# Kernel tuning notes

Hardware: AMD Instinct MI355X
Metric: run time of the kernel (lower is better)

The kernel has to match this reference:

```python
import jax, jax.numpy as jnp
import numpy as np

EMBED_DIM = 1024


def setup_inputs() -> dict:
    key = jax.random.key(0)
    ks = jax.random.split(key, 7)
    B, S, D = 4, 2048, EMBED_DIM
    scale = 1.0 / np.sqrt(D)
    x = jax.random.normal(ks[0], (B, S, D), dtype=jnp.float32)
    # nn.Linear weights stored as [out, in]; we keep [in, out] for x @ W
    Wq = jax.random.normal(ks[1], (D, D), dtype=jnp.float32) * scale
    bq = jax.random.normal(ks[2], (D,), dtype=jnp.float32) * scale
    Wk = jax.random.normal(ks[3], (D, D), dtype=jnp.float32) * scale
    bk = jax.random.normal(ks[4], (D,), dtype=jnp.float32) * scale
    Wv = jax.random.normal(ks[5], (D, D), dtype=jnp.float32) * scale
    bv = jax.random.normal(ks[6], (D,), dtype=jnp.float32) * scale
    return {"x": x, "Wq": Wq, "bq": bq, "Wk": Wk, "bk": bk, "Wv": Wv, "bv": bv}


def reference(x, Wq, bq, Wk, bk, Wv, bv):
    # Single-head attention (num_heads unused in original module).
    q = x @ Wq + bq            # [B, S, D]
    k = x @ Wk + bk            # [B, S, D]
    v = x @ Wv + bv            # [B, S, D]
    inv_sqrt_d = 1.0 / jnp.sqrt(jnp.asarray(x.shape[-1], x.dtype))
    scores = jnp.einsum("bsd,btd->bst", q, k) * inv_sqrt_d  # [B, S, S]
    attn = jax.nn.softmax(scores, axis=-1)
    return jnp.einsum("bst,btd->bsd", attn, v)
```

## Files before the change

kernel.cpp:

```cpp
#include <hip/hip_runtime.h>
#include <hip/hip_bf16.h>


using floatx4 = __attribute__((ext_vector_type(4))) float;
using shortx8 = __attribute__((ext_vector_type(8))) short;
using shortx4 = __attribute__((ext_vector_type(4))) short;

__device__ __forceinline__ short f2bf(float f) {
    __hip_bfloat16 h = __float2bfloat16(f);
    return *reinterpret_cast<short*>(&h);
}
__device__ __forceinline__ float bf2f(short s) {
    unsigned u = (unsigned)(unsigned short)s << 16;
    return __uint_as_float(u);
}

#define MFMA16(a, b, c) __builtin_amdgcn_mfma_f32_16x16x32_bf16((a), (b), (c), 0, 0, 0)

__device__ __forceinline__ void gld_lds16(const void* g, void* l) {
    __builtin_amdgcn_global_load_lds(
        (const __attribute__((address_space(1))) void*)g,
        (__attribute__((address_space(3))) void*)l, 16, 0, 0);
}

template<int MH>
__device__ __forceinline__ void rdA(const short* sAb, int wm, int lrow,
                                    int xo0, int xo1, shortx8 (&af)[4][2]) {
    const short* base = sAb + ((wm << 7) + (MH << 6) + lrow) * 64;
#pragma unroll
    for (int i = 0; i < 4; ++i) {
        af[i][0] = *reinterpret_cast<const shortx8*>(base + i * 1024 + xo0);
        af[i][1] = *reinterpret_cast<const shortx8*>(base + i * 1024 + xo1);
    }
}
template<int NH>
__device__ __forceinline__ void rdB(const short* sBb, int wn, int lrow,
                                    int xo0, int xo1, shortx8 (&bf)[4][2]) {
    const short* base = sBb + ((wn << 6) + (NH << 5) + lrow) * 64;
#pragma unroll
    for (int j = 0; j < 2; ++j) {
        bf[NH * 2 + j][0] = *reinterpret_cast<const shortx8*>(base + j * 1024 + xo0);
        bf[NH * 2 + j][1] = *reinterpret_cast<const shortx8*>(base + j * 1024 + xo1);
    }
}
template<int MH, int NH>
__device__ __forceinline__ void mfq(shortx8 (&af)[4][2], shortx8 (&bf)[4][2],
                                    floatx4 (&acc)[8][4]) {
    __builtin_amdgcn_s_setprio(1);
#pragma unroll
    for (int i = 0; i < 4; ++i) {
#pragma unroll
        for (int j = 0; j < 2; ++j) {
            acc[MH * 4 + i][NH * 2 + j] =
                MFMA16(af[i][0], bf[NH * 2 + j][0], acc[MH * 4 + i][NH * 2 + j]);
            acc[MH * 4 + i][NH * 2 + j] =
                MFMA16(af[i][1], bf[NH * 2 + j][1], acc[MH * 4 + i][NH * 2 + j]);
        }
    }
    __builtin_amdgcn_s_setprio(0);
}

__device__ __forceinline__ void gemm256_loop8(
    const short* __restrict__ A, const short* __restrict__ B,
    int lda, int ldb, int K,
    short* sA, short* sB, floatx4 (&acc)[8][4], int t)
{
    const int w = t >> 6, l = t & 63;
    const int wm = w >> 2, wn = w & 3;
    const int lrow = l & 15, quad = l >> 4, r8 = lrow & 7;
    const int xo0 = (quad ^ r8) << 3;
    const int xo1 = ((quad + 4) ^ r8) << 3;
    const int rr = t >> 3;
    const int gsw = ((t & 7) ^ (rr & 7)) << 3;
    const short* gA0 = A + (size_t)rr * lda + gsw;
    const short* gA1 = A + (size_t)(128 + rr) * lda + gsw;
    const short* gB0 = B + (size_t)rr * ldb + gsw;
    const short* gB1 = B + (size_t)(128 + rr) * ldb + gsw;
    const int wofs = w << 9;

    auto stage = [&](const short* g, int ld, int kt, short* ldsb) {
        const short* p = g + kt;
        gld_lds16(p, ldsb + wofs);
        gld_lds16(p + (size_t)(ld << 6), ldsb + wofs + 4096);
    };

    shortx8 af[4][2], bf[4][2];
    const int NT = K >> 6;

    stage(gA0, lda, 0, sA);
    stage(gA1, lda, 0, sA + 8192);
    stage(gB0, ldb, 0, sB);
    stage(gB1, ldb, 0, sB + 8192);
    stage(gB0, ldb, 64, sB + 16384);
    stage(gB1, ldb, 64, sB + 16384 + 8192);
    asm volatile("s_waitcnt vmcnt(4)" ::: "memory");
    __builtin_amdgcn_s_barrier();

    for (int T = 0; T < NT; T += 2) {
        const bool more = (T + 2) < NT;
        const int ktA1 = (T + 1) << 6;
        const int ktN2 = (T + 2) << 6;
        const int ktB3 = (T + 3) << 6;
        short* sA0 = sA;           short* sB0 = sB;
        short* sA1 = sA + 16384;   short* sB1 = sB + 16384;

        rdA<0>(sA0, wm, lrow, xo0, xo1, af);
        rdB<0>(sB0, wn, lrow, xo0, xo1, bf);
        stage(gA0, lda, ktA1, sA1);
        asm volatile("s_waitcnt lgkmcnt(8)" ::: "memory");
        __builtin_amdgcn_s_barrier();
        asm volatile("s_waitcnt lgkmcnt(0)" ::: "memory");
        __builtin_amdgcn_sched_barrier(0);
        mfq<0, 0>(af, bf, acc);
        __builtin_amdgcn_s_barrier();
        rdB<1>(sB0, wn, lrow, xo0, xo1, bf);
        stage(gA1, lda, ktA1, sA1 + 8192);
        __builtin_amdgcn_s_barrier();
        asm volatile("s_waitcnt lgkmcnt(0)" ::: "memory");
        __builtin_amdgcn_sched_barrier(0);
        mfq<0, 1>(af, bf, acc);
        __builtin_amdgcn_s_barrier();
        rdA<1>(sA0, wm, lrow, xo0, xo1, af);
        if (more) stage(gB0, ldb, ktN2, sB0);
        __builtin_amdgcn_s_barrier();
        asm volatile("s_waitcnt lgkmcnt(0)" ::: "memory");
        __builtin_amdgcn_sched_barrier(0);
        mfq<1, 0>(af, bf, acc);
        __builtin_amdgcn_s_barrier();
        if (more) stage(gB1, ldb, ktN2, sB0 + 8192);
        __builtin_amdgcn_s_barrier();
        __builtin_amdgcn_sched_barrier(0);
        mfq<1, 1>(af, bf, acc);
        if (more) { asm volatile("s_waitcnt vmcnt(4)" ::: "memory"); }
        else      { asm volatile("s_waitcnt vmcnt(0)" ::: "memory"); }
        __builtin_amdgcn_s_barrier();

        rdA<0>(sA1, wm, lrow, xo0, xo1, af);
        rdB<0>(sB1, wn, lrow, xo0, xo1, bf);
        if (more) stage(gA0, lda, ktN2, sA0);
        asm volatile("s_waitcnt lgkmcnt(8)" ::: "memory");
        __builtin_amdgcn_s_barrier();
        asm volatile("s_waitcnt lgkmcnt(0)" ::: "memory");
        __builtin_amdgcn_sched_barrier(0);
        mfq<0, 0>(af, bf, acc);
        __builtin_amdgcn_s_barrier();
        rdB<1>(sB1, wn, lrow, xo0, xo1, bf);
        if (more) stage(gA1, lda, ktN2, sA0 + 8192);
        __builtin_amdgcn_s_barrier();
        asm volatile("s_waitcnt lgkmcnt(0)" ::: "memory");
        __builtin_amdgcn_sched_barrier(0);
        mfq<0, 1>(af, bf, acc);
        __builtin_amdgcn_s_barrier();
        rdA<1>(sA1, wm, lrow, xo0, xo1, af);
        if (more) stage(gB0, ldb, ktB3, sB1);
        __builtin_amdgcn_s_barrier();
        asm volatile("s_waitcnt lgkmcnt(0)" ::: "memory");
        __builtin_amdgcn_sched_barrier(0);
        mfq<1, 0>(af, bf, acc);
        __builtin_amdgcn_s_barrier();
        if (more) stage(gB1, ldb, ktB3, sB1 + 8192);
        __builtin_amdgcn_s_barrier();
        __builtin_amdgcn_sched_barrier(0);
        mfq<1, 1>(af, bf, acc);
        if (more) { asm volatile("s_waitcnt vmcnt(4)" ::: "memory"); }
        __builtin_amdgcn_s_barrier();
    }
}

__device__ __forceinline__ void gemm_loop(
    const short* __restrict__ A, const short* __restrict__ B,
    size_t lda, size_t ldb, int K,
    short* as_, short* bs_, floatx4 (&acc)[4][4], int w, int l)
{
    const int lr8 = l >> 3;
    const int swz = ((l & 7) ^ lr8) * 8;
    const int lrow = l & 15, quad = l >> 4;
    const int wr = w >> 1, wc = w & 1;
    const int r8r = lrow & 7;
    const short* pa = A + (size_t)(w * 32 + lr8) * lda + swz;
    const short* pb = B + (size_t)(w * 32 + lr8) * ldb + swz;
    short* la = as_ + w * 4 * 512;
    short* lb = bs_ + w * 4 * 512;

    for (int kt = 0; kt < K; kt += 64) {
        for (int c = 0; c < 4; ++c) {
            gld_lds16(pa + (size_t)c * 8 * lda + kt, la + c * 512);
            gld_lds16(pb + (size_t)c * 8 * ldb + kt, lb + c * 512);
        }
        __syncthreads();
        for (int kk = 0; kk < 64; kk += 32) {
            const int xoff = (((kk >> 3) + quad) ^ r8r) << 3;
            shortx8 af[4], bfr[4];
            for (int i = 0; i < 4; ++i)
                af[i] = *reinterpret_cast<const shortx8*>(
                    &as_[(size_t)(wr * 64 + i * 16 + lrow) * 64 + xoff]);
            for (int j = 0; j < 4; ++j)
                bfr[j] = *reinterpret_cast<const shortx8*>(
                    &bs_[(size_t)(wc * 64 + j * 16 + lrow) * 64 + xoff]);
            for (int i = 0; i < 4; ++i)
                for (int j = 0; j < 4; ++j)
                    acc[i][j] = MFMA16(af[i], bfr[j], acc[i][j]);
        }
        __syncthreads();
    }
}

__global__ __launch_bounds__(256) void prep_kernel(
    const float* __restrict__ X,
    const float* __restrict__ Wq, const float* __restrict__ Wk,
    const float* __restrict__ Wv,
    const float* __restrict__ bq, const float* __restrict__ bk,
    const float* __restrict__ bv,
    short* __restrict__ Xb, short* __restrict__ Wt,
    float* __restrict__ bcat, float* __restrict__ sums)
{
    const int id = blockIdx.x, t = threadIdx.x;
    if (id < 4096) {
        size_t i = ((size_t)id * 256 + t) * 8;
        float4 v0 = *reinterpret_cast<const float4*>(X + i);
        float4 v1 = *reinterpret_cast<const float4*>(X + i + 4);
        shortx8 s;
        s[0] = f2bf(v0.x); s[1] = f2bf(v0.y); s[2] = f2bf(v0.z); s[3] = f2bf(v0.w);
        s[4] = f2bf(v1.x); s[5] = f2bf(v1.y); s[6] = f2bf(v1.z); s[7] = f2bf(v1.w);
        *reinterpret_cast<shortx8*>(Xb + i) = s;
    } else if (id < 4864) {
        __shared__ float tl[64][65];
        const int wid = id - 4096;
        const int z = wid >> 8, t16 = wid & 255;
        const float* src = (z == 0) ? Wq : (z == 1) ? Wk : Wv;
        short* dst = Wt + (size_t)z * 1024 * 1024;
        const int k0 = (t16 >> 4) * 64, n0 = (t16 & 15) * 64;
        for (int i = t; i < 64 * 64; i += 256) {
            int r = i >> 6, c = i & 63;
            tl[r][c] = src[(size_t)(k0 + r) * 1024 + n0 + c];
        }
        __syncthreads();
        for (int i = t; i < 64 * 64; i += 256) {
            int r = i >> 6, c = i & 63;
            dst[(size_t)(n0 + r) * 1024 + k0 + c] = f2bf(tl[c][r]);
        }
    } else if (id < 4867) {
        const int z = id - 4864;
        const float* bsrc = (z == 0) ? bq : (z == 1) ? bk : bv;
        for (int i = t; i < 1024; i += 256) bcat[z * 1024 + i] = bsrc[i];
    } else {
        const int sid = id - 4867;
        *reinterpret_cast<float4*>(&sums[sid * 1024 + t * 4]) =
            float4{0.f, 0.f, 0.f, 0.f};
    }
}

__global__ __launch_bounds__(512, 2) void qkv_qk_kernel(
    const short* __restrict__ Xb, const short* __restrict__ Wt,
    const float* __restrict__ bcat, short* __restrict__ dQ,
    short* __restrict__ dK)
{
    __shared__ short sA[2 * 16384];
    __shared__ short sB[2 * 16384];
    const int t = threadIdx.x;
    const int m0 = blockIdx.x * 256, n0 = blockIdx.y * 256;
    const int w = t >> 6, l = t & 63;
    const int wm = w >> 2, wn = w & 3, lrow = l & 15, quad = l >> 4;
    const int sec = n0 >> 10;

    floatx4 acc[8][4];
#pragma unroll
    for (int i = 0; i < 8; ++i)
#pragma unroll
        for (int j = 0; j < 4; ++j) acc[i][j] = floatx4{0.f, 0.f, 0.f, 0.f};

    gemm256_loop8(Xb + (size_t)m0 * 1024, Wt + (size_t)n0 * 1024,
                  1024, 1024, 1024, sA, sB, acc, t);

    short* outN = (sec == 0) ? dQ : dK;
#pragma unroll
    for (int i = 0; i < 8; ++i) {
        int rbase = m0 + wm * 128 + i * 16 + quad * 4;
#pragma unroll
        for (int j = 0; j < 4; ++j) {
            int coln = n0 + wn * 64 + j * 16 + lrow;
            int col = coln & 1023;
            float bvv = bcat[coln];
#pragma unroll
            for (int r = 0; r < 4; ++r)
                outN[(size_t)(rbase + r) * 1024 + col] =
                    f2bf(acc[i][j][r] + bvv);
        }
    }
}

__global__ __launch_bounds__(256) void qkv_v_kernel(
    const short* __restrict__ Xb, const short* __restrict__ Wt,
    const float* __restrict__ bcat, short* __restrict__ Vt)
{
    __shared__ short as_[128 * 64];
    __shared__ short bs_[128 * 64];
    const int t = threadIdx.x, w = t >> 6, l = t & 63;
    const int m0 = blockIdx.x * 128;
    const int n0 = 2048 + blockIdx.y * 128;
    const int wr = w >> 1, wc = w & 1, lrow = l & 15, quad = l >> 4;

    floatx4 acc[4][4];
    for (int i = 0; i < 4; ++i)
        for (int j = 0; j < 4; ++j) acc[i][j] = floatx4{0.f, 0.f, 0.f, 0.f};

    gemm_loop(Xb + (size_t)m0 * 1024, Wt + (size_t)n0 * 1024,
              1024, 1024, 1024, as_, bs_, acc, w, l);

    for (int i = 0; i < 4; ++i) {
        int rbase = m0 + wr * 64 + i * 16 + quad * 4;
        int b = rbase >> 11, sl = rbase & 2047;
        for (int j = 0; j < 4; ++j) {
            int coln = n0 + wc * 64 + j * 16 + lrow;
            int col = coln & 1023;
            float bvv = bcat[coln];
            shortx4 s;
            for (int r = 0; r < 4; ++r) s[r] = f2bf(acc[i][j][r] + bvv);
            *reinterpret_cast<shortx4*>(
                &Vt[((size_t)b * 1024 + col) * 2048 + sl]) = s;
        }
    }
}

__global__ __launch_bounds__(512, 2) void scores_kernel(
    const short* __restrict__ dQ, const short* __restrict__ dK,
    short* __restrict__ P, float* __restrict__ sums, int row_start)
{
    __shared__ short sA[2 * 16384];
    __shared__ short sB[2 * 16384];
    const int t = threadIdx.x;
    const int m0 = blockIdx.x * 256;
    const int n0 = blockIdx.y * 256;
    const int g0 = row_start + m0;
    const int b = g0 >> 11;
    const int w = t >> 6, l = t & 63;
    const int wm = w >> 2, wn = w & 3, lrow = l & 15, quad = l >> 4;

    floatx4 acc[8][4];
#pragma unroll
    for (int i = 0; i < 8; ++i)
#pragma unroll
        for (int j = 0; j < 4; ++j) acc[i][j] = floatx4{0.f, 0.f, 0.f, 0.f};

    gemm256_loop8(dQ + (size_t)g0 * 1024, dK + ((size_t)b * 2048 + n0) * 1024,
                  1024, 1024, 1024, sA, sB, acc, t);

#pragma unroll
    for (int i = 0; i < 8; ++i) {
        int rloc = m0 + wm * 128 + i * 16 + quad * 4;
        float rs[4] = {0.f, 0.f, 0.f, 0.f};
#pragma unroll
        for (int j = 0; j < 4; ++j) {
            int col = n0 + wn * 64 + j * 16 + lrow;
#pragma unroll
            for (int r = 0; r < 4; ++r) {
                short pb = f2bf(__expf(acc[i][j][r] * 0.03125f - 20.0f));
                P[(size_t)(rloc + r) * 2048 + col] = pb;
                rs[r] += bf2f(pb);
            }
        }
#pragma unroll
        for (int r = 0; r < 4; ++r)
            for (int m = 1; m <= 8; m <<= 1)
                rs[r] += __shfl_xor(rs[r], m, 64);
        if (lrow == 0)
#pragma unroll
            for (int r = 0; r < 4; ++r)
                atomicAdd(&sums[row_start + rloc + r], rs[r]);
    }
}

__global__ __launch_bounds__(256) void pv_kernel(
    const short* __restrict__ P, const short* __restrict__ Vt,
    const float* __restrict__ sums, float* __restrict__ Out, int row_start)
{
    __shared__ short as_[128 * 64];
    __shared__ short bs_[128 * 64];
    const int t = threadIdx.x, w = t >> 6, l = t & 63;
    const int m0 = blockIdx.x * 128;
    const int n0 = blockIdx.y * 128;
    const int g0 = row_start + m0;
    const int b = g0 >> 11;
    const int wr = w >> 1, wc = w & 1, lrow = l & 15, quad = l >> 4;

    floatx4 acc[4][4];
    for (int i = 0; i < 4; ++i)
        for (int j = 0; j < 4; ++j) acc[i][j] = floatx4{0.f, 0.f, 0.f, 0.f};

    gemm_loop(P + (size_t)m0 * 2048, Vt + ((size_t)b * 1024 + n0) * 2048,
              2048, 2048, 2048, as_, bs_, acc, w, l);

    for (int i = 0; i < 4; ++i) {
        int rloc = m0 + wr * 64 + i * 16 + quad * 4;
        int rglb = row_start + rloc;
        float is[4];
        for (int r = 0; r < 4; ++r) is[r] = 1.0f / sums[rglb + r];
        for (int j = 0; j < 4; ++j) {
            int col = n0 + wc * 64 + j * 16 + lrow;
            for (int r = 0; r < 4; ++r)
                Out[(size_t)(rglb + r) * 1024 + col] = acc[i][j][r] * is[r];
        }
    }
}

extern "C" void kernel_launch(void* const* d_in, const int* in_sizes, int n_in,
                              void* d_out, int out_size, void* d_ws, size_t ws_size,
                              hipStream_t stream)
{
    const float* x  = (const float*)d_in[0];
    const float* Wq = (const float*)d_in[1];
    const float* bq = (const float*)d_in[2];
    const float* Wk = (const float*)d_in[3];
    const float* bk = (const float*)d_in[4];
    const float* Wv = (const float*)d_in[5];
    const float* bv = (const float*)d_in[6];
    float* out = (float*)d_out;

    short* dQ = (short*)d_out;
    short* dK = dQ + (size_t)8192 * 1024;

    char* ws = (char*)d_ws;
    short* Wt   = (short*)ws;
    float* bcat = (float*)(ws + 6291456);
    float* sums = (float*)(ws + 6291456 + 12288);
    short* Vt   = (short*)(ws + 6291456 + 12288 + 32768);
    char*  region = ws + 6291456 + 12288 + 32768 + 16777216;
    const size_t base = 6291456 + 12288 + 32768 + 16777216;

    size_t avail = ws_size > base ? ws_size - base : 0;
    long rows_fit = (long)(avail / 4096);
    int chunk = (int)(rows_fit & ~255L);
    if (chunk > 8192) chunk = 8192;
    if (chunk < 256) chunk = 256;
    short* Xb = (short*)region;
    short* P  = (short*)region;

    prep_kernel<<<dim3(4875), 256, 0, stream>>>(x, Wq, Wk, Wv, bq, bk, bv,
                                                Xb, Wt, bcat, sums);
    qkv_qk_kernel<<<dim3(32, 8), 512, 0, stream>>>(Xb, Wt, bcat, dQ, dK);
    qkv_v_kernel<<<dim3(64, 8), 256, 0, stream>>>(Xb, Wt, bcat, Vt);

    for (int rs = 0; rs < 8192; rs += chunk) {
        int rows = 8192 - rs;
        if (rows > chunk) rows = chunk;
        scores_kernel<<<dim3(rows / 256, 8), 512, 0, stream>>>(dQ, dK, P, sums, rs);
        pv_kernel<<<dim3(rows / 128, 8), 256, 0, stream>>>(P, Vt, sums, out, rs);
    }
}
```

Baseline: 243.1 us.

## Replace atomic row sums with per-tile partials and remap blocks for XCD locality

Row-sum atomics in the scores kernel are replaced by an LDS reduction that writes one partial per column tile, and the PV kernel sums the 8 partials itself, so the prep kernel no longer zeroes the sums buffer. Both scores and PV kernels remap block indices when the grid is full size so that blocks sharing a batch land on the same XCD (blockIdx modulo 8), aiming for better L2 reuse of K/Vt. This costs a larger partials buffer and extra reads in the PV epilogue, and reuses sA as scratch after the GEMM loop.

```diff
diff --git a/kernel.cpp b/kernel.cpp
--- a/kernel.cpp
+++ b/kernel.cpp
@@ -212,7 +212,7 @@
     const float* __restrict__ bq, const float* __restrict__ bk,
     const float* __restrict__ bv,
     short* __restrict__ Xb, short* __restrict__ Wt,
-    float* __restrict__ bcat, float* __restrict__ sums)
+    float* __restrict__ bcat)
 {
     const int id = blockIdx.x, t = threadIdx.x;
     if (id < 4096) {
@@ -239,14 +239,10 @@
             int r = i >> 6, c = i & 63;
             dst[(size_t)(n0 + r) * 1024 + k0 + c] = f2bf(tl[c][r]);
         }
-    } else if (id < 4867) {
+    } else {
         const int z = id - 4864;
         const float* bsrc = (z == 0) ? bq : (z == 1) ? bk : bv;
         for (int i = t; i < 1024; i += 256) bcat[z * 1024 + i] = bsrc[i];
-    } else {
-        const int sid = id - 4867;
-        *reinterpret_cast<float4*>(&sums[sid * 1024 + t * 4]) =
-            float4{0.f, 0.f, 0.f, 0.f};
     }
 }
 
@@ -324,13 +320,21 @@
 
 __global__ __launch_bounds__(512, 2) void scores_kernel(
     const short* __restrict__ dQ, const short* __restrict__ dK,
-    short* __restrict__ P, float* __restrict__ sums, int row_start)
+    short* __restrict__ P, float* __restrict__ partials, int row_start)
 {
     __shared__ short sA[2 * 16384];
     __shared__ short sB[2 * 16384];
     const int t = threadIdx.x;
-    const int m0 = blockIdx.x * 256;
-    const int n0 = blockIdx.y * 256;
+    int bx = blockIdx.x, by = blockIdx.y;
+    if (gridDim.x == 32) {
+        const int c = bx & 7;
+        const int k = (bx >> 3) + (by << 2);
+        const int bb = c >> 1, half = c & 1;
+        bx = bb * 8 + (k & 3) + 4 * half;
+        by = k >> 2;
+    }
+    const int m0 = bx * 256;
+    const int n0 = by * 256;
     const int g0 = row_start + m0;
     const int b = g0 >> 11;
     const int w = t >> 6, l = t & 63;
@@ -345,9 +349,11 @@
     gemm256_loop8(dQ + (size_t)g0 * 1024, dK + ((size_t)b * 2048 + n0) * 1024,
                   1024, 1024, 1024, sA, sB, acc, t);
 
+    float* sred = reinterpret_cast<float*>(sA);
 #pragma unroll
     for (int i = 0; i < 8; ++i) {
-        int rloc = m0 + wm * 128 + i * 16 + quad * 4;
+        int rl = wm * 128 + i * 16 + quad * 4;
+        int rloc = m0 + rl;
         float rs[4] = {0.f, 0.f, 0.f, 0.f};
 #pragma unroll
         for (int j = 0; j < 4; ++j) {
@@ -366,19 +372,32 @@
         if (lrow == 0)
 #pragma unroll
             for (int r = 0; r < 4; ++r)
-                atomicAdd(&sums[row_start + rloc + r], rs[r]);
+                sred[(rl + r) * 4 + wn] = rs[r];
+    }
+    __syncthreads();
+    if (t < 256) {
+        float s = sred[t * 4] + sred[t * 4 + 1] + sred[t * 4 + 2] + sred[t * 4 + 3];
+        partials[(size_t)(row_start + m0 + t) * 8 + by] = s;
     }
 }
 
 __global__ __launch_bounds__(256) void pv_kernel(
     const short* __restrict__ P, const short* __restrict__ Vt,
-    const float* __restrict__ sums, float* __restrict__ Out, int row_start)
+    const float* __restrict__ partials, float* __restrict__ Out, int row_start)
 {
     __shared__ short as_[128 * 64];
     __shared__ short bs_[128 * 64];
     const int t = threadIdx.x, w = t >> 6, l = t & 63;
-    const int m0 = blockIdx.x * 128;
-    const int n0 = blockIdx.y * 128;
+    int bx = blockIdx.x, by = blockIdx.y;
+    if (gridDim.x == 64) {
+        const int c = bx & 7;
+        const int k = (bx >> 3) + (by << 3);
+        const int bb = c >> 1, half = c & 1;
+        bx = bb * 16 + (k & 7) + 8 * half;
+        by = k >> 3;
+    }
+    const int m0 = bx * 128;
+    const int n0 = by * 128;
     const int g0 = row_start + m0;
     const int b = g0 >> 11;
     const int wr = w >> 1, wc = w & 1, lrow = l & 15, quad = l >> 4;
@@ -394,7 +413,14 @@
         int rloc = m0 + wr * 64 + i * 16 + quad * 4;
         int rglb = row_start + rloc;
         float is[4];
-        for (int r = 0; r < 4; ++r) is[r] = 1.0f / sums[rglb + r];
+        for (int r = 0; r < 4; ++r) {
+            const float4* pp =
+                reinterpret_cast<const float4*>(&partials[(size_t)(rglb + r) * 8]);
+            float4 p0 = pp[0], p1 = pp[1];
+            float s = (p0.x + p0.y) + (p0.z + p0.w) +
+                      (p1.x + p1.y) + (p1.z + p1.w);
+            is[r] = 1.0f / s;
+        }
         for (int j = 0; j < 4; ++j) {
             int col = n0 + wc * 64 + j * 16 + lrow;
             for (int r = 0; r < 4; ++r)
@@ -422,10 +448,10 @@
     char* ws = (char*)d_ws;
     short* Wt   = (short*)ws;
     float* bcat = (float*)(ws + 6291456);
-    float* sums = (float*)(ws + 6291456 + 12288);
-    short* Vt   = (short*)(ws + 6291456 + 12288 + 32768);
-    char*  region = ws + 6291456 + 12288 + 32768 + 16777216;
-    const size_t base = 6291456 + 12288 + 32768 + 16777216;
+    float* partials = (float*)(ws + 6291456 + 12288);
+    short* Vt   = (short*)(ws + 6291456 + 12288 + 262144);
+    char*  region = ws + 6291456 + 12288 + 262144 + 16777216;
+    const size_t base = 6291456 + 12288 + 262144 + 16777216;
 
     size_t avail = ws_size > base ? ws_size - base : 0;
     long rows_fit = (long)(avail / 4096);
@@ -435,15 +461,15 @@
     short* Xb = (short*)region;
     short* P  = (short*)region;
 
-    prep_kernel<<<dim3(4875), 256, 0, stream>>>(x, Wq, Wk, Wv, bq, bk, bv,
-                                                Xb, Wt, bcat, sums);
+    prep_kernel<<<dim3(4867), 256, 0, stream>>>(x, Wq, Wk, Wv, bq, bk, bv,
+                                                Xb, Wt, bcat);
     qkv_qk_kernel<<<dim3(32, 8), 512, 0, stream>>>(Xb, Wt, bcat, dQ, dK);
     qkv_v_kernel<<<dim3(64, 8), 256, 0, stream>>>(Xb, Wt, bcat, Vt);
 
     for (int rs = 0; rs < 8192; rs += chunk) {
         int rows = 8192 - rs;
         if (rows > chunk) rows = chunk;
-        scores_kernel<<<dim3(rows / 256, 8), 512, 0, stream>>>(dQ, dK, P, sums, rs);
-        pv_kernel<<<dim3(rows / 128, 8), 256, 0, stream>>>(P, Vt, sums, out, rs);
-    }
-}
+        scores_kernel<<<dim3(rows / 256, 8), 512, 0, stream>>>(dQ, dK, P, partials, rs);
+        pv_kernel<<<dim3(rows / 128, 8), 256, 0, stream>>>(P, Vt, partials, out, rs);
+    }
+}
```

Result: faster. 230.4 us (-5.2%).
